# Kernel optimization log

Hardware: AMD Instinct MI355X
Metric: run time of the kernel (lower is better)

Reference implementation:

```python
import jax, jax.numpy as jnp
import numpy as np

EMBED_DIM = 1024
NUM_HEADS = 16
HEAD_DIM = EMBED_DIM // NUM_HEADS
SCALING = HEAD_DIM ** -0.5
EPS = 1e-5


def _rope(seq_len):
    inv_freq = 1.0 / (10000.0 ** (jnp.arange(0, HEAD_DIM, 2, dtype=jnp.float32) / HEAD_DIM))
    freqs = jnp.arange(seq_len, dtype=jnp.float32)[:, None] * inv_freq[None, :]
    emb = jnp.concatenate([freqs, freqs], axis=-1)  # (S, HEAD_DIM)
    return jnp.cos(emb), jnp.sin(emb)


def _rotate(x, cos, sin):
    # x: (B,H,S,Dh), cos/sin: (S,Dh)
    d = x.shape[-1]
    x1, x2 = x[..., : d // 2], x[..., d // 2 :]
    rotated = jnp.concatenate([-x2, x1], axis=-1)
    return x * cos + rotated * sin


def setup_inputs() -> dict:
    key = jax.random.key(0)
    ks = jax.random.split(key, 6)
    B, S, D = 2, 2048, EMBED_DIM
    scale = D ** -0.5
    return {
        "x": jax.random.normal(ks[0], (B, S, D), jnp.float32),
        "Wq": jax.random.normal(ks[1], (D, D), jnp.float32) * scale,
        "Wk": jax.random.normal(ks[2], (D, D), jnp.float32) * scale,
        "Wv": jax.random.normal(ks[3], (D, D), jnp.float32) * scale,
        "Wg": jax.random.normal(ks[4], (D, D), jnp.float32) * scale,
        "Wo": jax.random.normal(ks[5], (D, D), jnp.float32) * scale,
        "gn_w": jnp.ones((D,), jnp.float32),
        "gn_b": jnp.zeros((D,), jnp.float32),
    }


def reference(x, Wq, Wk, Wv, Wg, Wo, gn_w, gn_b):
    B, S, D = x.shape
    H, Dh = NUM_HEADS, HEAD_DIM

    def split_heads(t):  # (B,S,D) -> (B,H,S,Dh)
        return t.reshape(B, S, H, Dh).transpose(0, 2, 1, 3)

    q = split_heads(x @ Wq.T)
    k = split_heads(x @ Wk.T)
    v = split_heads(x @ Wv.T)

    cos, sin = _rope(S)
    q = _rotate(q, cos, sin)
    k = _rotate(k, cos, sin)

    retention = jnp.einsum("bhsd,bhtd->bhst", q, k) * SCALING

    # multiplicative causal decay mask: gamma**(n-m) for n>=m else 0
    gammas = (1.0 - 2.0 ** (-5.0 - jnp.arange(H, dtype=jnp.float32)))  # (H,)
    diff = jnp.arange(S)[:, None] - jnp.arange(S)[None, :]             # (S,S)
    causal = diff >= 0
    decay = jnp.where(causal, gammas[:, None, None] ** jnp.maximum(diff, 0).astype(jnp.float32), 0.0)  # (H,S,S)
    retention = retention * decay[None]

    out = jnp.einsum("bhst,bhtd->bhsd", retention, v)  # (B,H,S,Dh)
    out = out.transpose(0, 2, 1, 3).reshape(B * S, H, Dh)

    # GroupNorm with num_groups == H over channel dim D
    mean = out.mean(axis=-1, keepdims=True)
    var = out.var(axis=-1, keepdims=True)
    out = (out - mean) * jax.lax.rsqrt(var + EPS)
    out = out * gn_w.reshape(H, Dh) + gn_b.reshape(H, Dh)
    out = out.reshape(B, S, D)

    gate = jax.nn.silu(x @ Wg.T)
    return (gate * out) @ Wo.T
```

## Files before the change

kernel.cpp:

```cpp
#include <hip/hip_runtime.h>
#include <cstdint>
#include <cstddef>


typedef __attribute__((ext_vector_type(4))) float  f32x4;
typedef __attribute__((ext_vector_type(8))) short  bf16x8;
typedef __attribute__((ext_vector_type(4))) short  bf16x4v;
typedef __attribute__((ext_vector_type(2))) unsigned int u32x2;

#define MFMA_BF16 __builtin_amdgcn_mfma_f32_16x16x32_bf16

#define GLL16(gp, lp) __builtin_amdgcn_global_load_lds( \
    (const __attribute__((address_space(1))) unsigned int*)(const void*)(gp), \
    (__attribute__((address_space(3))) unsigned int*)(void*)(lp), 16, 0, 0)

__device__ __forceinline__ unsigned short f2bf(float f) {
    unsigned u = __float_as_uint(f);
    u += 0x7fffu + ((u >> 16) & 1u);
    return (unsigned short)(u >> 16);
}
__device__ __forceinline__ float bf2f(unsigned short h) {
    return __uint_as_float(((unsigned)h) << 16);
}
__device__ __forceinline__ unsigned cvt_pk_bf16(float lo, float hi) {
    unsigned r;
    asm("v_cvt_pk_bf16_f32 %0, %1, %2" : "=v"(r) : "v"(lo), "v"(hi));
    return r;
}

__global__ void convert_kernel(const float* __restrict__ x,
                               const float* __restrict__ wq, const float* __restrict__ wk,
                               const float* __restrict__ wv, const float* __restrict__ wg,
                               const float* __restrict__ wo,
                               unsigned short* __restrict__ dst,
                               float* __restrict__ cosT, float* __restrict__ sinT) {
    const size_t total = 4194304u + 5u * 1048576u;
    for (size_t i = (size_t)blockIdx.x * blockDim.x + threadIdx.x;
         i * 4 < total; i += (size_t)gridDim.x * blockDim.x) {
        size_t e = i * 4;
        const float* src; size_t off;
        if (e < 4194304u) { src = x; off = e; }
        else {
            size_t r = e - 4194304u;
            int w = (int)(r >> 20); off = r & 1048575u;
            src = (w == 0) ? wq : (w == 1) ? wk : (w == 2) ? wv : (w == 3) ? wg : wo;
        }
        f32x4 v = *(const f32x4*)(src + off);
        unsigned short o0 = f2bf(v[0]), o1 = f2bf(v[1]), o2 = f2bf(v[2]), o3 = f2bf(v[3]);
        unsigned long long pack = (unsigned long long)o0 | ((unsigned long long)o1 << 16)
                                | ((unsigned long long)o2 << 32) | ((unsigned long long)o3 << 48);
        *(unsigned long long*)(dst + e) = pack;
    }
    if (blockIdx.x < 256) {
        int i = blockIdx.x * 256 + threadIdx.x;
        int s = i >> 5, j = i & 31;
        float inv = exp2f(-(float)j * (13.287712379549449f / 32.0f));
        float ang = (float)s * inv;
        cosT[i] = cosf(ang);
        sinT[i] = sinf(ang);
    }
}

__launch_bounds__(256, 2)
__global__ void gemm_fused(const unsigned short* __restrict__ A_x,
                           const unsigned short* __restrict__ A_a2,
                           const unsigned short* __restrict__ Wq, const unsigned short* __restrict__ Wk,
                           const unsigned short* __restrict__ Wv, const unsigned short* __restrict__ Wg,
                           const unsigned short* __restrict__ Wo,
                           const float* __restrict__ cosT, const float* __restrict__ sinT,
                           unsigned short* __restrict__ q_hm, unsigned short* __restrict__ k_hm,
                           unsigned short* __restrict__ kTs, unsigned short* __restrict__ vT,
                           unsigned short* __restrict__ gate,
                           float* __restrict__ outf,
                           int mode_base) {
    int mode = mode_base + blockIdx.z;
    const unsigned short* A = (mode == 4) ? A_a2 : A_x;
    const unsigned short* W = (mode == 0) ? Wq : (mode == 1) ? Wk :
                              (mode == 2) ? Wv : (mode == 3) ? Wg : Wo;

    __shared__ __align__(16) unsigned short Ash[2][128 * 64];
    __shared__ __align__(16) unsigned short Bsh[2][128 * 64];

    int tid = threadIdx.x;
    int lane = tid & 63, wid = tid >> 6;
    int wm = wid >> 1, wn = wid & 1;
    int m0 = blockIdx.y * 128, n0 = blockIdx.x * 128;

    int l_row = lane >> 3;
    int l_src = ((lane & 7) ^ l_row) << 3;
    const unsigned short* Ab = A + (size_t)(m0 + wid * 32 + l_row) * 1024 + l_src;
    const unsigned short* Wb = W + (size_t)(n0 + wid * 32 + l_row) * 1024 + l_src;

    f32x4 acc[4][4];
#pragma unroll
    for (int i = 0; i < 4; ++i)
#pragma unroll
        for (int j = 0; j < 4; ++j)
#pragma unroll
            for (int r = 0; r < 4; ++r) acc[i][j][r] = 0.0f;

#define STAGE(BUF, K0)                                                          \
    _Pragma("unroll")                                                           \
    for (int i_ = 0; i_ < 4; ++i_) {                                            \
        GLL16(Ab + (size_t)(i_ * 8) * 1024 + (K0), &Ash[BUF][(wid * 32 + i_ * 8) * 64]); \
        GLL16(Wb + (size_t)(i_ * 8) * 1024 + (K0), &Bsh[BUF][(wid * 32 + i_ * 8) * 64]); \
    }

#define COMPUTE(BUF)                                                            \
    _Pragma("unroll")                                                           \
    for (int ks = 0; ks < 2; ++ks) {                                            \
        bf16x8 af[4], bfv[4];                                                   \
        _Pragma("unroll")                                                       \
        for (int mi = 0; mi < 4; ++mi) {                                        \
            int row = wm * 64 + mi * 16 + (lane & 15);                          \
            int c = ks * 4 + (lane >> 4);                                       \
            af[mi] = *(const bf16x8*)&Ash[BUF][row * 64 + ((c ^ (row & 7)) << 3)]; \
        }                                                                       \
        _Pragma("unroll")                                                       \
        for (int ni = 0; ni < 4; ++ni) {                                        \
            int row = wn * 64 + ni * 16 + (lane & 15);                          \
            int c = ks * 4 + (lane >> 4);                                       \
            bfv[ni] = *(const bf16x8*)&Bsh[BUF][row * 64 + ((c ^ (row & 7)) << 3)]; \
        }                                                                       \
        __builtin_amdgcn_s_setprio(1);                                          \
        if (mode == 2) {                                \
            _Pragma("unroll")                                                   \
            for (int mi = 0; mi < 4; ++mi)                                      \
                _Pragma("unroll")                                               \
                for (int ni = 0; ni < 4; ++ni)                                  \
                    acc[mi][ni] = MFMA_BF16(bfv[ni], af[mi], acc[mi][ni], 0, 0, 0); \
        } else {                                                                \
            _Pragma("unroll")                                                   \
            for (int mi = 0; mi < 4; ++mi)                                      \
                _Pragma("unroll")                                               \
                for (int ni = 0; ni < 4; ++ni)                                  \
                    acc[mi][ni] = MFMA_BF16(af[mi], bfv[ni], acc[mi][ni], 0, 0, 0); \
        }                                                                       \
        __builtin_amdgcn_s_setprio(0);                                          \
    }

    STAGE(0, 0)
    asm volatile("s_waitcnt vmcnt(0)" ::: "memory");
    __syncthreads();

    for (int t = 0; t < 15; ++t) {
        int cur = t & 1;
        STAGE(cur ^ 1, (t + 1) * 64)
        COMPUTE(cur)
        asm volatile("s_waitcnt vmcnt(0)" ::: "memory");
        __syncthreads();
    }
    COMPUTE(1)

#undef STAGE
#undef COMPUTE

    int mbase = m0 + wm * 64, nbase = n0 + wn * 64;
    int g4 = (lane >> 4) << 2;

    if (mode == 0 || mode == 1) {
        unsigned short* dst = (mode == 0) ? q_hm : k_hm;
        float sr[4] = {1.f, 1.f, 1.f, 1.f}, m16p[4] = {1.f, 1.f, 1.f, 1.f};
        if (mode == 1) {
            float lg = log2f(1.0f - exp2f(-5.0f - (float)(nbase >> 6)));
            float gm1 = exp2f(-lg), gm16 = exp2f(-16.0f * lg);
            sr[0] = exp2f(lg * (float)(63 - g4));
            sr[1] = sr[0] * gm1; sr[2] = sr[1] * gm1; sr[3] = sr[2] * gm1;
            m16p[1] = gm16; m16p[2] = gm16 * gm16; m16p[3] = m16p[2] * gm16;
        }
#pragma unroll
        for (int mi = 0; mi < 4; ++mi)
#pragma unroll
            for (int ni = 0; ni < 4; ++ni)
#pragma unroll
                for (int r = 0; r < 4; ++r) {
                    int m = mbase + mi * 16 + g4 + r;
                    int n = nbase + ni * 16 + (lane & 15);
                    int s = m & 2047, b = m >> 11, h = n >> 6, d = n & 63, j = d & 31;
                    float v  = acc[mi][ni][r];
                    float v2 = acc[mi][ni ^ 2][r];
                    float cs = cosT[s * 32 + j], sn = sinT[s * 32 + j];
                    float rot = (d < 32) ? -v2 : v2;
                    float o = v * cs + rot * sn;
                    dst[((size_t)(b * 16 + h) * 2048 + s) * 64 + d] = f2bf(o);
                    if (mode == 1) {
                        kTs[((size_t)((b * 16 + h) * 64 + d)) * 2048 + s]
                            = f2bf(o * (sr[r] * m16p[mi]));
                    }
                }
    } else if (mode == 2) {
#pragma unroll
        for (int mi = 0; mi < 4; ++mi)
#pragma unroll
            for (int ni = 0; ni < 4; ++ni)
#pragma unroll
                for (int r = 0; r < 4; ++r) {
                    int n = nbase + ni * 16 + g4 + r;
                    int m = mbase + mi * 16 + (lane & 15);
                    int b = m >> 11, s = m & 2047, h = n >> 6, d = n & 63;
                    vT[((size_t)((b * 16 + h) * 64 + d)) * 2048 + s] = f2bf(acc[mi][ni][r]);
                }
    } else if (mode == 3) {
#pragma unroll
        for (int mi = 0; mi < 4; ++mi)
#pragma unroll
            for (int ni = 0; ni < 4; ++ni)
#pragma unroll
                for (int r = 0; r < 4; ++r) {
                    int m = mbase + mi * 16 + g4 + r;
                    int n = nbase + ni * 16 + (lane & 15);
                    float v = acc[mi][ni][r];
                    gate[(size_t)m * 1024 + n] = f2bf(v / (1.0f + expf(-v)));
                }
    } else {
#pragma unroll
        for (int mi = 0; mi < 4; ++mi)
#pragma unroll
            for (int ni = 0; ni < 4; ++ni)
#pragma unroll
                for (int r = 0; r < 4; ++r) {
                    int m = mbase + mi * 16 + g4 + r;
                    int n = nbase + ni * 16 + (lane & 15);
                    outf[(size_t)m * 1024 + n] = acc[mi][ni][r];
                }
    }
}

__launch_bounds__(256, 4)
__global__ void chunk_state_kernel(const unsigned short* __restrict__ vT,
                                   const unsigned short* __restrict__ kTs,
                                   unsigned short* __restrict__ LT) {
    int tid = threadIdx.x, lane = tid & 63, wid = tid >> 6;
    int bh = blockIdx.x >> 3;
    int c  = (blockIdx.x & 7) * 4 + wid;
    int q_lane = lane & 15;
    int g4 = (lane >> 4) << 2, g8 = (lane >> 4) << 3;

    const unsigned short* vb = vT  + (size_t)bh * 131072 + (size_t)c * 64;
    const unsigned short* kb = kTs + (size_t)bh * 131072 + (size_t)c * 64;

    f32x4 acc[4][4];
#pragma unroll
    for (int i = 0; i < 4; ++i)
#pragma unroll
        for (int j = 0; j < 4; ++j)
#pragma unroll
            for (int r = 0; r < 4; ++r) acc[i][j][r] = 0.0f;

#pragma unroll
    for (int ks = 0; ks < 2; ++ks) {
        bf16x8 a[4], bv[4];
#pragma unroll
        for (int mi = 0; mi < 4; ++mi)
            a[mi] = *(const bf16x8*)(vb + (size_t)(mi * 16 + q_lane) * 2048 + ks * 32 + g8);
#pragma unroll
        for (int ni = 0; ni < 4; ++ni)
            bv[ni] = *(const bf16x8*)(kb + (size_t)(ni * 16 + q_lane) * 2048 + ks * 32 + g8);
#pragma unroll
        for (int mi = 0; mi < 4; ++mi)
#pragma unroll
            for (int ni = 0; ni < 4; ++ni)
                acc[mi][ni] = MFMA_BF16(a[mi], bv[ni], acc[mi][ni], 0, 0, 0);
    }

    unsigned short* lp = LT + ((size_t)(bh * 32 + c)) * 4096;
#pragma unroll
    for (int mi = 0; mi < 4; ++mi)
#pragma unroll
        for (int ni = 0; ni < 4; ++ni)
#pragma unroll
            for (int r = 0; r < 4; ++r) {
                int d2 = mi * 16 + g4 + r;
                int d1 = ni * 16 + q_lane;
                lp[d2 * 64 + d1] = f2bf(acc[mi][ni][r]);
            }
}

__launch_bounds__(256, 4)
__global__ void scan_kernel(const unsigned short* __restrict__ LT,
                            unsigned short* __restrict__ ST) {
    int bh = blockIdx.x >> 2;
    int e0 = ((blockIdx.x & 3) * 256 + threadIdx.x) * 4;
    int h = bh & 15;
    float lg2g = log2f(1.0f - exp2f(-5.0f - (float)h));
    float g64 = exp2f(64.0f * lg2g);

    float s0 = 0.f, s1 = 0.f, s2 = 0.f, s3 = 0.f;
    const unsigned short* lp = LT + (size_t)bh * 32 * 4096 + e0;
    unsigned short* sp = ST + (size_t)bh * 32 * 4096 + e0;
    for (int c = 0; c < 32; ++c) {
        u32x2 wv;
        wv[0] = cvt_pk_bf16(s0, s1);
        wv[1] = cvt_pk_bf16(s2, s3);
        *(u32x2*)sp = wv;
        bf16x4v lv = *(const bf16x4v*)lp;
        s0 = s0 * g64 + bf2f((unsigned short)lv[0]);
        s1 = s1 * g64 + bf2f((unsigned short)lv[1]);
        s2 = s2 * g64 + bf2f((unsigned short)lv[2]);
        s3 = s3 * g64 + bf2f((unsigned short)lv[3]);
        lp += 4096; sp += 4096;
    }
}

__launch_bounds__(256, 4)
__global__ void retention_chunk_kernel(const unsigned short* __restrict__ qh,
                                       const unsigned short* __restrict__ kh,
                                       const unsigned short* __restrict__ vT,
                                       const unsigned short* __restrict__ ST,
                                       const float* __restrict__ gn_w, const float* __restrict__ gn_b,
                                       const unsigned short* __restrict__ gate,
                                       unsigned short* __restrict__ a2) {
    __shared__ __align__(16) unsigned short Ssh[4][16 * 40];

    int tid = threadIdx.x, lane = tid & 63, wid = tid >> 6;
    int c = blockIdx.x, bh = blockIdx.y;
    int b = bh >> 4, h = bh & 15;

    float lg2g = log2f(1.0f - exp2f(-5.0f - (float)h));
    float gam1 = exp2f(lg2g);
    float gmr1 = exp2f(-lg2g);
    float gmr2 = gmr1 * gmr1, gmr3 = gmr2 * gmr1;
    float gmr16 = exp2f(-16.0f * lg2g);

    int q_lane = lane & 15;
    int g4 = (lane >> 4) << 2, g8 = (lane >> 4) << 3;
    int i_col = wid * 16 + q_lane;
    int s_abs = c * 64 + i_col;

    bf16x8 aq0, aq1;
    {
        const unsigned short* qp = qh + ((size_t)bh * 2048 + s_abs) * 64 + g8;
        aq0 = *(const bf16x8*)(qp);
        aq1 = *(const bf16x8*)(qp + 32);
    }

    f32x4 z4 = {0.f, 0.f, 0.f, 0.f};
    f32x4 o0, o1, o2, o3;

    {
        const unsigned short* stp = ST + ((size_t)(bh * 32 + c)) * 4096
                                  + (size_t)q_lane * 64 + g8;
        bf16x8 s00 = *(const bf16x8*)(stp);
        bf16x8 s01 = *(const bf16x8*)(stp + 32);
        bf16x8 s10 = *(const bf16x8*)(stp + 1024);
        bf16x8 s11 = *(const bf16x8*)(stp + 1056);
        bf16x8 s20 = *(const bf16x8*)(stp + 2048);
        bf16x8 s21 = *(const bf16x8*)(stp + 2080);
        bf16x8 s30 = *(const bf16x8*)(stp + 3072);
        bf16x8 s31 = *(const bf16x8*)(stp + 3104);
        o0 = MFMA_BF16(aq0, s00, z4, 0, 0, 0); o0 = MFMA_BF16(aq1, s01, o0, 0, 0, 0);
        o1 = MFMA_BF16(aq0, s10, z4, 0, 0, 0); o1 = MFMA_BF16(aq1, s11, o1, 0, 0, 0);
        o2 = MFMA_BF16(aq0, s20, z4, 0, 0, 0); o2 = MFMA_BF16(aq1, s21, o2, 0, 0, 0);
        o3 = MFMA_BF16(aq0, s30, z4, 0, 0, 0); o3 = MFMA_BF16(aq1, s31, o3, 0, 0, 0);
    }
    {
        float cs0 = 0.125f * exp2f(lg2g * (float)(wid * 16 + g4 + 1));
        float cs1 = cs0 * gam1, cs2 = cs1 * gam1, cs3 = cs2 * gam1;
        o0[0] *= cs0; o0[1] *= cs1; o0[2] *= cs2; o0[3] *= cs3;
        o1[0] *= cs0; o1[1] *= cs1; o1[2] *= cs2; o1[3] *= cs3;
        o2[0] *= cs0; o2[1] *= cs1; o2[2] *= cs2; o2[3] *= cs3;
        o3[0] *= cs0; o3[1] *= cs1; o3[2] *= cs2; o3[3] *= cs3;
    }

    const unsigned short* kbase = kh + ((size_t)bh * 2048 + c * 64) * 64;
    const unsigned short* vbase = vT + (size_t)bh * 131072 + c * 64;
    unsigned short* ssw = &Ssh[wid][0];
    int ntt = (wid >> 1) + 1;
    for (int tt = 0; tt < ntt; ++tt) {
        int tbase = tt * 32;
        const unsigned short* kp = kbase + (size_t)(tbase + q_lane) * 64 + g8;
        bf16x8 k00 = *(const bf16x8*)(kp);
        bf16x8 k01 = *(const bf16x8*)(kp + 32);
        bf16x8 k10 = *(const bf16x8*)(kp + 1024);
        bf16x8 k11 = *(const bf16x8*)(kp + 1056);
        f32x4 sc0 = z4, sc1 = z4;
        sc0 = MFMA_BF16(k00, aq0, sc0, 0, 0, 0);
        sc0 = MFMA_BF16(k01, aq1, sc0, 0, 0, 0);
        sc1 = MFMA_BF16(k10, aq0, sc1, 0, 0, 0);
        sc1 = MFMA_BF16(k11, aq1, sc1, 0, 0, 0);

        int j0 = tbase + g4;
        float e0 = 0.125f * exp2f(lg2g * (float)(i_col - j0));
        float e1 = e0 * gmr1, e2 = e0 * gmr2, e3 = e0 * gmr3;
        float v00 = (i_col >= j0    ) ? sc0[0] * e0 : 0.0f;
        float v01 = (i_col >= j0 + 1) ? sc0[1] * e1 : 0.0f;
        float v02 = (i_col >= j0 + 2) ? sc0[2] * e2 : 0.0f;
        float v03 = (i_col >= j0 + 3) ? sc0[3] * e3 : 0.0f;
        int j1 = j0 + 16;
        float f0 = e0 * gmr16, f1 = e1 * gmr16, f2 = e2 * gmr16, f3 = e3 * gmr16;
        float v10 = (i_col >= j1    ) ? sc1[0] * f0 : 0.0f;
        float v11 = (i_col >= j1 + 1) ? sc1[1] * f1 : 0.0f;
        float v12 = (i_col >= j1 + 2) ? sc1[2] * f2 : 0.0f;
        float v13 = (i_col >= j1 + 3) ? sc1[3] * f3 : 0.0f;

        u32x2 wA, wB;
        wA[0] = cvt_pk_bf16(v00, v01); wA[1] = cvt_pk_bf16(v02, v03);
        wB[0] = cvt_pk_bf16(v10, v11); wB[1] = cvt_pk_bf16(v12, v13);
        *(u32x2*)&ssw[q_lane * 40 + g4] = wA;
        *(u32x2*)&ssw[q_lane * 40 + 16 + g4] = wB;

        bf16x8 sf = *(const bf16x8*)&ssw[q_lane * 40 + g8];
        bf16x8 bv0 = *(const bf16x8*)(vbase + (size_t)(q_lane) * 2048 + tbase + g8);
        bf16x8 bv1 = *(const bf16x8*)(vbase + (size_t)(16 + q_lane) * 2048 + tbase + g8);
        bf16x8 bv2 = *(const bf16x8*)(vbase + (size_t)(32 + q_lane) * 2048 + tbase + g8);
        bf16x8 bv3 = *(const bf16x8*)(vbase + (size_t)(48 + q_lane) * 2048 + tbase + g8);
        o0 = MFMA_BF16(sf, bv0, o0, 0, 0, 0);
        o1 = MFMA_BF16(sf, bv1, o1, 0, 0, 0);
        o2 = MFMA_BF16(sf, bv2, o2, 0, 0, 0);
        o3 = MFMA_BF16(sf, bv3, o3, 0, 0, 0);
    }

    float mean[4], rstd[4];
#pragma unroll
    for (int r = 0; r < 4; ++r) {
        float s1 = o0[r] + o1[r] + o2[r] + o3[r];
        float s2 = o0[r]*o0[r] + o1[r]*o1[r] + o2[r]*o2[r] + o3[r]*o3[r];
#pragma unroll
        for (int m = 1; m < 16; m <<= 1) {
            s1 += __shfl_xor(s1, m);
            s2 += __shfl_xor(s2, m);
        }
        float mu = s1 * 0.015625f;
        mean[r] = mu;
        float var = s2 * 0.015625f - mu * mu;
        rstd[r] = rsqrtf(var + 1e-5f);
    }
    int srow = c * 64 + wid * 16;
#define RT_STORE(OV, DB)                                                    \
    {                                                                       \
        int d = DB * 16 + q_lane;                                           \
        float gw = gn_w[h * 64 + d];                                        \
        float gb = gn_b[h * 64 + d];                                        \
        _Pragma("unroll")                                                   \
        for (int r = 0; r < 4; ++r) {                                       \
            int s_out = srow + g4 + r;                                      \
            size_t gi = ((size_t)(b * 2048 + s_out)) * 1024 + h * 64 + d;   \
            float val = (OV[r] - mean[r]) * rstd[r] * gw + gb;              \
            val *= bf2f(gate[gi]);                                          \
            a2[gi] = f2bf(val);                                             \
        }                                                                   \
    }
    RT_STORE(o0, 0); RT_STORE(o1, 1); RT_STORE(o2, 2); RT_STORE(o3, 3);
#undef RT_STORE
}

extern "C" void kernel_launch(void* const* d_in, const int* in_sizes, int n_in,
                              void* d_out, int out_size, void* d_ws, size_t ws_size,
                              hipStream_t stream) {
    const float* x    = (const float*)d_in[0];
    const float* Wq   = (const float*)d_in[1];
    const float* Wk   = (const float*)d_in[2];
    const float* Wv   = (const float*)d_in[3];
    const float* Wg   = (const float*)d_in[4];
    const float* Wo   = (const float*)d_in[5];
    const float* gn_w = (const float*)d_in[6];
    const float* gn_b = (const float*)d_in[7];

    unsigned short* xb   = (unsigned short*)d_ws;
    unsigned short* wqb  = xb  + 4194304;
    unsigned short* wkb  = wqb + 1048576;
    unsigned short* wvb  = wkb + 1048576;
    unsigned short* wgb  = wvb + 1048576;
    unsigned short* wob  = wgb + 1048576;
    float*          cosT = (float*)(wob + 1048576);
    float*          sinT = cosT + 65536;
    unsigned short* q_hm = (unsigned short*)(sinT + 65536);
    unsigned short* k_hm = q_hm + 4194304;
    unsigned short* vTb  = k_hm + 4194304;
    unsigned short* kTs  = vTb + 4194304;
    unsigned short* a2   = kTs + 4194304;
    unsigned short* gate = a2  + 4194304;
    unsigned short* LT   = a2;
    unsigned short* ST   = xb;

    float* outf = (float*)d_out;

    convert_kernel<<<dim3(2048), dim3(256), 0, stream>>>(
        x, Wq, Wk, Wv, Wg, Wo, xb, cosT, sinT);
    gemm_fused<<<dim3(8, 32, 4), dim3(256), 0, stream>>>(
        xb, a2, wqb, wkb, wvb, wgb, wob, cosT, sinT,
        q_hm, k_hm, kTs, vTb, gate, outf, 0);
    chunk_state_kernel<<<dim3(256), dim3(256), 0, stream>>>(vTb, kTs, LT);
    scan_kernel<<<dim3(128), dim3(256), 0, stream>>>(LT, ST);
    retention_chunk_kernel<<<dim3(32, 32), dim3(256), 0, stream>>>(
        q_hm, k_hm, vTb, ST, gn_w, gn_b, gate, a2);
    gemm_fused<<<dim3(8, 32, 1), dim3(256), 0, stream>>>(
        xb, a2, wqb, wkb, wvb, wgb, wob, cosT, sinT,
        q_hm, k_hm, kTs, vTb, gate, outf, 4);
}
```

Measured before the change: 120.2 us.

## Use four-stage LDS ring with half-depth K tiles and partial vmcnt waits

The GEMM main loop changes from a double-buffered 64-wide K tile to a four-buffer ring of 32-wide K tiles, keeping the same LDS footprint. It prefetches three tiles ahead and waits only for the oldest tile's loads with s_waitcnt vmcnt(8) plus a raw s_barrier, instead of draining all loads each iteration. The LDS XOR swizzle is redone for 64-byte rows. The goal is to hide global-load latency behind more in-flight stages. The cost is twice as many barriers and half as many MFMAs between each sync.

Measured after the change: 134.6 us. 12.0% more time.

```diff
diff --git a/kernel.cpp b/kernel.cpp
--- a/kernel.cpp
+++ b/kernel.cpp
@@ -78,18 +78,18 @@
     const unsigned short* W = (mode == 0) ? Wq : (mode == 1) ? Wk :
                               (mode == 2) ? Wv : (mode == 3) ? Wg : Wo;
 
-    __shared__ __align__(16) unsigned short Ash[2][128 * 64];
-    __shared__ __align__(16) unsigned short Bsh[2][128 * 64];
+    __shared__ __align__(16) unsigned short Ash[4][128 * 32];
+    __shared__ __align__(16) unsigned short Bsh[4][128 * 32];
 
     int tid = threadIdx.x;
     int lane = tid & 63, wid = tid >> 6;
     int wm = wid >> 1, wn = wid & 1;
     int m0 = blockIdx.y * 128, n0 = blockIdx.x * 128;
 
-    int l_row = lane >> 3;
-    int l_src = ((lane & 7) ^ l_row) << 3;
-    const unsigned short* Ab = A + (size_t)(m0 + wid * 32 + l_row) * 1024 + l_src;
-    const unsigned short* Wb = W + (size_t)(n0 + wid * 32 + l_row) * 1024 + l_src;
+    int r16  = lane >> 2;
+    int csw  = ((lane & 3) ^ ((r16 >> 1) & 3)) << 3;
+    const unsigned short* Ab = A + (size_t)(m0 + wid * 32 + r16) * 1024 + csw;
+    const unsigned short* Wb = W + (size_t)(n0 + wid * 32 + r16) * 1024 + csw;
 
     f32x4 acc[4][4];
 #pragma unroll
@@ -99,28 +99,30 @@
 #pragma unroll
             for (int r = 0; r < 4; ++r) acc[i][j][r] = 0.0f;
 
-#define STAGE(BUF, K0)                                                          \
-    _Pragma("unroll")                                                           \
-    for (int i_ = 0; i_ < 4; ++i_) {                                            \
-        GLL16(Ab + (size_t)(i_ * 8) * 1024 + (K0), &Ash[BUF][(wid * 32 + i_ * 8) * 64]); \
-        GLL16(Wb + (size_t)(i_ * 8) * 1024 + (K0), &Bsh[BUF][(wid * 32 + i_ * 8) * 64]); \
+#define STAGE(BUF, T)                                                           \
+    {                                                                           \
+        int k0_ = (T) * 32;                                                     \
+        GLL16(Ab + k0_,               &Ash[BUF][(wid * 32) * 32]);              \
+        GLL16(Ab + 16 * 1024 + k0_,   &Ash[BUF][(wid * 32 + 16) * 32]);         \
+        GLL16(Wb + k0_,               &Bsh[BUF][(wid * 32) * 32]);              \
+        GLL16(Wb + 16 * 1024 + k0_,   &Bsh[BUF][(wid * 32 + 16) * 32]);         \
     }
 
 #define COMPUTE(BUF)                                                            \
-    _Pragma("unroll")                                                           \
-    for (int ks = 0; ks < 2; ++ks) {                                            \
+    {                                                                           \
         bf16x8 af[4], bfv[4];                                                   \
+        int c_ = lane >> 4;                                                     \
         _Pragma("unroll")                                                       \
         for (int mi = 0; mi < 4; ++mi) {                                        \
             int row = wm * 64 + mi * 16 + (lane & 15);                          \
-            int c = ks * 4 + (lane >> 4);                                       \
-            af[mi] = *(const bf16x8*)&Ash[BUF][row * 64 + ((c ^ (row & 7)) << 3)]; \
+            af[mi] = *(const bf16x8*)&Ash[BUF][row * 32 +                       \
+                                      ((c_ ^ ((row >> 1) & 3)) << 3)];          \
         }                                                                       \
         _Pragma("unroll")                                                       \
         for (int ni = 0; ni < 4; ++ni) {                                        \
             int row = wn * 64 + ni * 16 + (lane & 15);                          \
-            int c = ks * 4 + (lane >> 4);                                       \
-            bfv[ni] = *(const bf16x8*)&Bsh[BUF][row * 64 + ((c ^ (row & 7)) << 3)]; \
+            bfv[ni] = *(const bf16x8*)&Bsh[BUF][row * 32 +                      \
+                                       ((c_ ^ ((row >> 1) & 3)) << 3)];         \
         }                                                                       \
         __builtin_amdgcn_s_setprio(1);                                          \
         if (mode == 2) {                                \
@@ -139,21 +141,27 @@
         __builtin_amdgcn_s_setprio(0);                                          \
     }
 
+#define WAITV(N) asm volatile("s_waitcnt vmcnt(" #N ")" ::: "memory")
+#define BARRIER  asm volatile("s_barrier" ::: "memory")
+
     STAGE(0, 0)
-    asm volatile("s_waitcnt vmcnt(0)" ::: "memory");
-    __syncthreads();
-
-    for (int t = 0; t < 15; ++t) {
-        int cur = t & 1;
-        STAGE(cur ^ 1, (t + 1) * 64)
-        COMPUTE(cur)
-        asm volatile("s_waitcnt vmcnt(0)" ::: "memory");
-        __syncthreads();
-    }
-    COMPUTE(1)
+    STAGE(1, 1)
+    STAGE(2, 2)
+
+    for (int t = 0; t < 29; ++t) {
+        WAITV(8);
+        BARRIER;
+        STAGE((t + 3) & 3, t + 3)
+        COMPUTE(t & 3)
+    }
+    WAITV(8); BARRIER; COMPUTE(1)
+    WAITV(4); BARRIER; COMPUTE(2)
+    WAITV(0); BARRIER; COMPUTE(3)
 
 #undef STAGE
 #undef COMPUTE
+#undef WAITV
+#undef BARRIER
 
     int mbase = m0 + wm * 64, nbase = n0 + wn * 64;
     int g4 = (lane >> 4) << 2;
```
